# Kernel tuning notes

Hardware: AMD Instinct MI355X
Metric: run time of the kernel (lower is better)

## Reference

```python
import jax, jax.numpy as jnp
import numpy as np

N_NODES = 50000
N_EDGES = 600000
FEAT = 128
HID = 256


def _sage_gcn(feats, src, dst, W, b, n_nodes):
    # DGL SAGEConv aggregator_type='gcn':
    # h_neigh = (sum_{u in N(v)} h_u + h_v) / (in_deg(v) + 1); out = h_neigh @ W + b
    neigh_sum = jax.ops.segment_sum(feats[src], dst, num_segments=n_nodes)  # [N, d]
    in_deg = jax.ops.segment_sum(jnp.ones((src.shape[0],), feats.dtype), dst,
                                 num_segments=n_nodes)  # [N]
    h = (neigh_sum + feats) / (in_deg + 1.0)[:, None]
    return h @ W + b


def setup_inputs() -> dict:
    key = jax.random.key(0)
    ks = jax.random.split(key, 8)
    s = lambda d: 1.0 / np.sqrt(d)
    return {
        "features": jax.random.normal(ks[0], (N_NODES, FEAT), jnp.float32),
        "src": jax.random.randint(ks[1], (N_EDGES,), 0, N_NODES, jnp.int32),
        "dst": jax.random.randint(ks[2], (N_EDGES,), 0, N_NODES, jnp.int32),
        "W1": jax.random.normal(ks[3], (FEAT, HID), jnp.float32) * s(FEAT),
        "b1": jnp.zeros((HID,), jnp.float32),
        "W2": jax.random.normal(ks[4], (HID, HID), jnp.float32) * s(HID),
        "b2": jnp.zeros((HID,), jnp.float32),
        "Wd1": jax.random.normal(ks[5], (HID, HID), jnp.float32) * s(HID),
        "bd1": jnp.zeros((HID,), jnp.float32),
        "Wd2": jax.random.normal(ks[6], (HID, 1), jnp.float32) * s(HID),
        "bd2": jnp.zeros((1,), jnp.float32),
    }


def reference(features, src, dst, W1, b1, W2, b2, Wd1, bd1, Wd2, bd2):
    n = features.shape[0]
    # Encoder: SAGEConv(gcn) -> ReLU -> SAGEConv(gcn)   (dropout inactive in eval)
    h = _sage_gcn(features, src, dst, W1, b1, n)
    h = jax.nn.relu(h)
    h = _sage_gcn(h, src, dst, W2, b2, n)
    # Decoder: Linear -> ReLU -> Linear
    h = jax.nn.relu(h @ Wd1 + bd1)
    return h @ Wd2 + bd2  # [N, 1]
```

## Files before the change

kernel.cpp:

```cpp
#include <hip/hip_runtime.h>
#include <type_traits>

#define NN 50000
#define NE 600000
#define FEAT 128
#define HID 256
#define MAXD 64

typedef float v4f __attribute__((ext_vector_type(4)));
typedef float f32x4 __attribute__((ext_vector_type(4)));
typedef __bf16 bf16x8 __attribute__((ext_vector_type(8)));
using u16 = unsigned short;
using u32 = unsigned int;
typedef u16 u16x4 __attribute__((ext_vector_type(4)));
typedef u16 u16x8 __attribute__((ext_vector_type(8)));

__device__ __forceinline__ u16 f2bf(float f) {
    u32 u = __builtin_bit_cast(u32, f);
    u += 0x7fffu + ((u >> 16) & 1u);
    return (u16)(u >> 16);
}
__device__ __forceinline__ float bf2f(u16 h) {
    u32 u = ((u32)h) << 16;
    return __builtin_bit_cast(float, u);
}

#define NB_FILL 2344
#define NB_CVT 6250
#define NB_W1  128
#define NB_W23 256
__global__ __launch_bounds__(256) void prep_fill_k(const int* __restrict__ src,
                                                   const int* __restrict__ dst,
                                                   int* __restrict__ cnt,
                                                   int* __restrict__ ell,
                                                   const float* __restrict__ feats,
                                                   const float* __restrict__ W1,
                                                   const float* __restrict__ W2,
                                                   const float* __restrict__ Wd1,
                                                   const float* __restrict__ b2,
                                                   u16* __restrict__ featsbf,
                                                   u16* __restrict__ WT1,
                                                   u16* __restrict__ WT23,
                                                   float* __restrict__ c23) {
    int b = blockIdx.x, t = threadIdx.x;
    if (b < NB_FILL) {
        int e = b * 256 + t;
        if (e < NE) {
            int d = dst[e];
            int p = atomicAdd(&cnt[d], 1);
            if (p < MAXD) ell[(size_t)d * MAXD + p] = src[e];
        }
        return;
    }
    b -= NB_FILL;
    if (b < NB_CVT) {
        int i = b * 256 + t;
        v4f v = *(const v4f*)(feats + (size_t)i * 4);
        u16x4 o;
        #pragma unroll
        for (int j = 0; j < 4; j++) o[j] = f2bf(v[j]);
        *(u16x4*)(featsbf + (size_t)i * 4) = o;
    } else if (b < NB_CVT + NB_W1) {
        int idx = (b - NB_CVT) * 256 + t;
        int k = idx >> 8, n = idx & 255;
        WT1[(size_t)n * 128 + k] = f2bf(W1[idx]);
    } else if (b < NB_CVT + NB_W1 + NB_W23) {
        int k = b - NB_CVT - NB_W1;
        int n = t;
        const float* w2row = W2 + (size_t)k * 256;
        float acc = 0.f;
        #pragma unroll 8
        for (int j = 0; j < 256; j++) acc += w2row[j] * Wd1[(size_t)j * 256 + n];
        WT23[(size_t)n * 256 + k] = f2bf(acc);
    } else {
        int n = t;
        float acc = 0.f;
        #pragma unroll 8
        for (int j = 0; j < 256; j++) acc += b2[j] * Wd1[(size_t)j * 256 + n];
        c23[n] = acc;
    }
}

template <int D>
__global__ __launch_bounds__(256) void aggregate_bf_k(const u16* __restrict__ x,
                                                      const int* __restrict__ cnt,
                                                      const int* __restrict__ ell,
                                                      u16* __restrict__ o) {
    constexpr int LPG = (D == 256) ? 32 : 16;
    constexpr int G = 64 / LPG;
    int wave = threadIdx.x >> 6;
    int lane = threadIdx.x & 63;
    int v = blockIdx.x * 4 + wave;
    if (v >= NN) return;
    int g  = lane / LPG;
    int li = lane & (LPG - 1);
    size_t coff = (size_t)li * 8;
    int deg = cnt[v]; if (deg > MAXD) deg = MAXD;
    int cntv = deg + 1;
    const int* cols = ell + (size_t)v * MAXD;
    float acc[8];
    #pragma unroll
    for (int i = 0; i < 8; i++) acc[i] = 0.f;
    int base = 0;
    #pragma unroll 4
    for (; base + G <= cntv; base += G) {
        int idx = base + g;
        int row = (idx < deg) ? cols[idx] : v;
        u16x8 r = *(const u16x8*)(x + (size_t)row * D + coff);
        #pragma unroll
        for (int i = 0; i < 8; i++) acc[i] += bf2f(r[i]);
    }
    if (base + g < cntv) {
        int idx = base + g;
        int row = (idx < deg) ? cols[idx] : v;
        u16x8 r = *(const u16x8*)(x + (size_t)row * D + coff);
        #pragma unroll
        for (int i = 0; i < 8; i++) acc[i] += bf2f(r[i]);
    }
    #pragma unroll
    for (int i = 0; i < 8; i++) {
        acc[i] += __shfl_xor(acc[i], 32, 64);
        if (G == 4) acc[i] += __shfl_xor(acc[i], 16, 64);
    }
    if (lane < LPG) {
        float inv = 1.0f / (float)cntv;
        u16x8 O;
        #pragma unroll
        for (int i = 0; i < 8; i++) O[i] = f2bf(acc[i] * inv);
        *(u16x8*)(o + (size_t)v * D + coff) = O;
    }
}

__global__ __launch_bounds__(256) void agg2_dec_k(const u16* __restrict__ x,
                                                  const int* __restrict__ cnt,
                                                  const int* __restrict__ ell,
                                                  const float* __restrict__ bd1,
                                                  const float* __restrict__ wd2,
                                                  const float* __restrict__ bd2,
                                                  float* __restrict__ out) {
    int wave = threadIdx.x >> 6;
    int lane = threadIdx.x & 63;
    int v = blockIdx.x * 4 + wave;
    if (v >= NN) return;
    int g  = lane >> 5;
    int li = lane & 31;
    size_t coff = (size_t)li * 8;
    int deg = cnt[v]; if (deg > MAXD) deg = MAXD;
    int cntv = deg + 1;
    const int* cols = ell + (size_t)v * MAXD;
    float acc[8];
    #pragma unroll
    for (int i = 0; i < 8; i++) acc[i] = 0.f;
    int base = 0;
    #pragma unroll 4
    for (; base + 2 <= cntv; base += 2) {
        int idx = base + g;
        int row = (idx < deg) ? cols[idx] : v;
        u16x8 r = *(const u16x8*)(x + (size_t)row * 256 + coff);
        #pragma unroll
        for (int i = 0; i < 8; i++) acc[i] += bf2f(r[i]);
    }
    if (base + g < cntv) {
        int idx = base + g;
        int row = (idx < deg) ? cols[idx] : v;
        u16x8 r = *(const u16x8*)(x + (size_t)row * 256 + coff);
        #pragma unroll
        for (int i = 0; i < 8; i++) acc[i] += bf2f(r[i]);
    }
    #pragma unroll
    for (int i = 0; i < 8; i++) acc[i] += __shfl_xor(acc[i], 32, 64);

    float inv = 1.0f / (float)cntv;
    v4f b0 = *(const v4f*)(bd1 + li * 8);
    v4f b1 = *(const v4f*)(bd1 + li * 8 + 4);
    v4f w0 = *(const v4f*)(wd2 + li * 8);
    v4f w1 = *(const v4f*)(wd2 + li * 8 + 4);
    float p = 0.f;
    #pragma unroll
    for (int i = 0; i < 4; i++) p += fmaxf(acc[i] * inv + b0[i], 0.f) * w0[i];
    #pragma unroll
    for (int i = 0; i < 4; i++) p += fmaxf(acc[i + 4] * inv + b1[i], 0.f) * w1[i];
    p += __shfl_xor(p, 1, 64);
    p += __shfl_xor(p, 2, 64);
    p += __shfl_xor(p, 4, 64);
    p += __shfl_xor(p, 8, 64);
    p += __shfl_xor(p, 16, 64);
    if (lane == 0) out[v] = p + bd2[0];
}

#define MFMA_BF16 __builtin_amdgcn_mfma_f32_16x16x32_bf16
#define SW(s, r) (((s) ^ (((r) >> 1) & 3)) * 8)

#define MFMA_STEP(pa0, pa1, pa2, pa3, ph0, ph1)              \
    do {                                                     \
        acc[0][0] = MFMA_BF16(pa0, ph0, acc[0][0], 0, 0, 0); \
        acc[0][1] = MFMA_BF16(pa0, ph1, acc[0][1], 0, 0, 0); \
        acc[1][0] = MFMA_BF16(pa1, ph0, acc[1][0], 0, 0, 0); \
        acc[1][1] = MFMA_BF16(pa1, ph1, acc[1][1], 0, 0, 0); \
        acc[2][0] = MFMA_BF16(pa2, ph0, acc[2][0], 0, 0, 0); \
        acc[2][1] = MFMA_BF16(pa2, ph1, acc[2][1], 0, 0, 0); \
        acc[3][0] = MFMA_BF16(pa3, ph0, acc[3][0], 0, 0, 0); \
        acc[3][1] = MFMA_BF16(pa3, ph1, acc[3][1], 0, 0, 0); \
    } while (0)

__global__ __launch_bounds__(512, 4) void fused_gemm12_k(const u16* __restrict__ A1,
                                                         const u16* __restrict__ B1,
                                                         const float* __restrict__ b1,
                                                         const u16* __restrict__ B23,
                                                         const float* __restrict__ c23,
                                                         u16* __restrict__ Z, int M) {
    __shared__ __attribute__((aligned(16))) u16 sA[2][64 * 32];
    __shared__ __attribute__((aligned(16))) u16 sB[2][256 * 32];
    __shared__ __attribute__((aligned(16))) u16 sH[64 * 264];

    int tid = threadIdx.x;
    int wid = tid >> 6, lane = tid & 63;
    int m0 = blockIdx.x * 64;
    int r16 = lane & 15, sl = lane >> 4, k8 = sl * 8;

    u32 ao[4], bo[2];
    #pragma unroll
    for (int mf = 0; mf < 4; mf++) {
        int ar = mf * 16 + r16;
        ao[mf] = ar * 32 + SW(sl, ar);
    }
    #pragma unroll
    for (int nf = 0; nf < 2; nf++) {
        int bc = wid * 32 + nf * 16 + r16;
        bo[nf] = bc * 32 + SW(sl, bc);
    }

    f32x4 acc[4][2];
    #pragma unroll
    for (int a = 0; a < 4; a++)
        #pragma unroll
        for (int b = 0; b < 2; b++) acc[a][b] = (f32x4)0.f;

    int aRow = tid >> 2, aS = tid & 3;
    u32 aSw = aRow * 32 + SW(aS, aRow);
    int gAr = m0 + aRow; if (gAr >= M) gAr = M - 1;
    const u16* gA = A1 + (size_t)gAr * 128 + aS * 8;
    int bRow[2], bS[2]; u32 bSw[2];
    #pragma unroll
    for (int j = 0; j < 2; j++) {
        int idx = tid + j * 512;
        bRow[j] = idx >> 2; bS[j] = idx & 3;
        bSw[j] = bRow[j] * 32 + SW(bS[j], bRow[j]);
    }

    uint4 rA, rB0, rB1;

    if (tid < 256) rA = *(const uint4*)gA;
    rB0 = *(const uint4*)(B1 + (size_t)bRow[0] * 128 + bS[0] * 8);
    rB1 = *(const uint4*)(B1 + (size_t)bRow[1] * 128 + bS[1] * 8);
    if (tid < 256) *(uint4*)(&sA[0][aSw]) = rA;
    *(uint4*)(&sB[0][bSw[0]]) = rB0;
    *(uint4*)(&sB[0][bSw[1]]) = rB1;
    __syncthreads();

    #pragma unroll
    for (int kb = 0; kb < 4; kb++) {
        int cur = kb & 1;
        if (kb < 3) {
            if (tid < 256) rA = *(const uint4*)(gA + (kb + 1) * 32);
            rB0 = *(const uint4*)(B1 + (size_t)bRow[0] * 128 + (kb + 1) * 32 + bS[0] * 8);
            rB1 = *(const uint4*)(B1 + (size_t)bRow[1] * 128 + (kb + 1) * 32 + bS[1] * 8);
        }
        bf16x8 a0 = *(const bf16x8*)(&sA[cur][ao[0]]);
        bf16x8 a1 = *(const bf16x8*)(&sA[cur][ao[1]]);
        bf16x8 a2 = *(const bf16x8*)(&sA[cur][ao[2]]);
        bf16x8 a3 = *(const bf16x8*)(&sA[cur][ao[3]]);
        bf16x8 h0 = *(const bf16x8*)(&sB[cur][bo[0]]);
        bf16x8 h1 = *(const bf16x8*)(&sB[cur][bo[1]]);
        MFMA_STEP(a0, a1, a2, a3, h0, h1);
        if (kb < 3) {
            int nxt = cur ^ 1;
            if (tid < 256) *(uint4*)(&sA[nxt][aSw]) = rA;
            *(uint4*)(&sB[nxt][bSw[0]]) = rB0;
            *(uint4*)(&sB[nxt][bSw[1]]) = rB1;
        }
        __syncthreads();
    }

    rB0 = *(const uint4*)(B23 + (size_t)bRow[0] * 256 + bS[0] * 8);
    rB1 = *(const uint4*)(B23 + (size_t)bRow[1] * 256 + bS[1] * 8);

    {
        float b1c[2];
        #pragma unroll
        for (int nf = 0; nf < 2; nf++) b1c[nf] = b1[wid * 32 + nf * 16 + r16];
        int rbase = sl * 4;
        #pragma unroll
        for (int mf = 0; mf < 4; mf++)
            #pragma unroll
            for (int j = 0; j < 4; j++) {
                int r = mf * 16 + rbase + j;
                #pragma unroll
                for (int nf = 0; nf < 2; nf++) {
                    int c = wid * 32 + nf * 16 + r16;
                    sH[r * 264 + c] = f2bf(fmaxf(acc[mf][nf][j] + b1c[nf], 0.f));
                }
            }
        #pragma unroll
        for (int a = 0; a < 4; a++)
            #pragma unroll
            for (int b = 0; b < 2; b++) acc[a][b] = (f32x4)0.f;
    }
    *(uint4*)(&sB[0][bSw[0]]) = rB0;
    *(uint4*)(&sB[0][bSw[1]]) = rB1;
    __syncthreads();

    #pragma unroll
    for (int kb = 0; kb < 8; kb++) {
        int cur = kb & 1;
        if (kb < 7) {
            rB0 = *(const uint4*)(B23 + (size_t)bRow[0] * 256 + (kb + 1) * 32 + bS[0] * 8);
            rB1 = *(const uint4*)(B23 + (size_t)bRow[1] * 256 + (kb + 1) * 32 + bS[1] * 8);
        }
        bf16x8 a0 = *(const bf16x8*)(sH + (0 * 16 + r16) * 264 + kb * 32 + k8);
        bf16x8 a1 = *(const bf16x8*)(sH + (1 * 16 + r16) * 264 + kb * 32 + k8);
        bf16x8 a2 = *(const bf16x8*)(sH + (2 * 16 + r16) * 264 + kb * 32 + k8);
        bf16x8 a3 = *(const bf16x8*)(sH + (3 * 16 + r16) * 264 + kb * 32 + k8);
        bf16x8 h0 = *(const bf16x8*)(&sB[cur][bo[0]]);
        bf16x8 h1 = *(const bf16x8*)(&sB[cur][bo[1]]);
        MFMA_STEP(a0, a1, a2, a3, h0, h1);
        if (kb < 7) {
            int nxt = cur ^ 1;
            *(uint4*)(&sB[nxt][bSw[0]]) = rB0;
            *(uint4*)(&sB[nxt][bSw[1]]) = rB1;
        }
        __syncthreads();
    }

    {
        float cc[2];
        #pragma unroll
        for (int nf = 0; nf < 2; nf++) cc[nf] = c23[wid * 32 + nf * 16 + r16];
        int rbase = sl * 4;
        #pragma unroll
        for (int mf = 0; mf < 4; mf++)
            #pragma unroll
            for (int j = 0; j < 4; j++) {
                int gr = m0 + mf * 16 + rbase + j;
                if (gr < M) {
                    #pragma unroll
                    for (int nf = 0; nf < 2; nf++) {
                        int gc = wid * 32 + nf * 16 + r16;
                        Z[(size_t)gr * 256 + gc] = f2bf(acc[mf][nf][j] + cc[nf]);
                    }
                }
            }
    }
}

extern "C" void kernel_launch(void* const* d_in, const int* in_sizes, int n_in,
                              void* d_out, int out_size, void* d_ws, size_t ws_size,
                              hipStream_t stream) {
    const float* feats = (const float*)d_in[0];
    const int*   src   = (const int*)d_in[1];
    const int*   dst   = (const int*)d_in[2];
    const float* W1    = (const float*)d_in[3];
    const float* b1    = (const float*)d_in[4];
    const float* W2    = (const float*)d_in[5];
    const float* b2    = (const float*)d_in[6];
    const float* Wd1   = (const float*)d_in[7];
    const float* bd1   = (const float*)d_in[8];
    const float* Wd2   = (const float*)d_in[9];
    const float* bd2   = (const float*)d_in[10];
    float* out = (float*)d_out;

    char* base = (char*)d_ws;
    size_t off = 0;
    int* cnt = (int*)(base + off); off += (size_t)NN * 4;
    int* ell = (int*)(base + off); off += (size_t)NN * MAXD * 4;
    u16* WT1   = (u16*)(base + off); off += (size_t)FEAT * 256 * 2;
    u16* WT23  = (u16*)(base + off); off += (size_t)HID * 256 * 2;
    float* c23 = (float*)(base + off); off += 256 * 4;
    off = (off + 255) & ~(size_t)255;
    u16* featsbf = (u16*)(base + off); off += (size_t)NN * FEAT * 2;
    u16* A1      = (u16*)(base + off); off += (size_t)NN * FEAT * 2;
    u16* Zbf     = (u16*)(base + off); off += (size_t)NN * HID * 2;

    hipMemsetAsync(cnt, 0, (size_t)NN * 4, stream);
    prep_fill_k<<<NB_FILL + NB_CVT + NB_W1 + NB_W23 + 1, 256, 0, stream>>>(
        src, dst, cnt, ell, feats, W1, W2, Wd1, b2, featsbf, WT1, WT23, c23);

    aggregate_bf_k<FEAT><<<(NN + 3) / 4, 256, 0, stream>>>(featsbf, cnt, ell, A1);

    fused_gemm12_k<<<(NN + 63) / 64, 512, 0, stream>>>(A1, WT1, b1, WT23, c23,
                                                       Zbf, NN);

    agg2_dec_k<<<(NN + 3) / 4, 256, 0, stream>>>(Zbf, cnt, ell, bd1, Wd2, bd2, out);
}
```

Measured before the change: 157.4 us.

## Store ELL neighbor indices as u16 and split W2·Wd1 fold into its own kernel

The ELL neighbor list is stored as 16-bit indices instead of 32-bit, which is valid because the node count fits in u16. This halves index traffic in the fill and in both aggregation kernels. The edge-fill blocks now handle 4 edges per thread. The W2·Wd1 weight fold moves out of the prep kernel into a dedicated kernel that stages 4 W2 rows in shared memory, so each Wd1 load is reused across 4 outputs. The trade-off is an extra kernel launch, and that fold no longer overlaps with the fill work.

```diff
diff --git a/kernel.cpp b/kernel.cpp
--- a/kernel.cpp
+++ b/kernel.cpp
@@ -25,30 +25,28 @@
     return __builtin_bit_cast(float, u);
 }
 
-#define NB_FILL 2344
+#define NB_FILL 586
 #define NB_CVT 6250
 #define NB_W1  128
-#define NB_W23 256
 __global__ __launch_bounds__(256) void prep_fill_k(const int* __restrict__ src,
                                                    const int* __restrict__ dst,
                                                    int* __restrict__ cnt,
-                                                   int* __restrict__ ell,
+                                                   u16* __restrict__ ell,
                                                    const float* __restrict__ feats,
                                                    const float* __restrict__ W1,
-                                                   const float* __restrict__ W2,
-                                                   const float* __restrict__ Wd1,
-                                                   const float* __restrict__ b2,
                                                    u16* __restrict__ featsbf,
-                                                   u16* __restrict__ WT1,
-                                                   u16* __restrict__ WT23,
-                                                   float* __restrict__ c23) {
+                                                   u16* __restrict__ WT1) {
     int b = blockIdx.x, t = threadIdx.x;
     if (b < NB_FILL) {
-        int e = b * 256 + t;
-        if (e < NE) {
-            int d = dst[e];
-            int p = atomicAdd(&cnt[d], 1);
-            if (p < MAXD) ell[(size_t)d * MAXD + p] = src[e];
+        int ebase = b * 1024 + t;
+        #pragma unroll
+        for (int i = 0; i < 4; i++) {
+            int e = ebase + i * 256;
+            if (e < NE) {
+                int d = dst[e];
+                int p = atomicAdd(&cnt[d], 1);
+                if (p < MAXD) ell[(size_t)d * MAXD + p] = (u16)src[e];
+            }
         }
         return;
     }
@@ -60,31 +58,43 @@
         #pragma unroll
         for (int j = 0; j < 4; j++) o[j] = f2bf(v[j]);
         *(u16x4*)(featsbf + (size_t)i * 4) = o;
-    } else if (b < NB_CVT + NB_W1) {
+    } else {
         int idx = (b - NB_CVT) * 256 + t;
         int k = idx >> 8, n = idx & 255;
         WT1[(size_t)n * 128 + k] = f2bf(W1[idx]);
-    } else if (b < NB_CVT + NB_W1 + NB_W23) {
-        int k = b - NB_CVT - NB_W1;
-        int n = t;
-        const float* w2row = W2 + (size_t)k * 256;
-        float acc = 0.f;
-        #pragma unroll 8
-        for (int j = 0; j < 256; j++) acc += w2row[j] * Wd1[(size_t)j * 256 + n];
-        WT23[(size_t)n * 256 + k] = f2bf(acc);
-    } else {
-        int n = t;
-        float acc = 0.f;
-        #pragma unroll 8
-        for (int j = 0; j < 256; j++) acc += b2[j] * Wd1[(size_t)j * 256 + n];
-        c23[n] = acc;
-    }
+    }
+}
+
+__global__ __launch_bounds__(256) void w23_k(const float* __restrict__ W2,
+                                             const float* __restrict__ Wd1,
+                                             const float* __restrict__ b2,
+                                             u16* __restrict__ WT23,
+                                             float* __restrict__ c23) {
+    __shared__ float w2s[4][256];
+    int t = threadIdx.x;
+    int k0 = blockIdx.x * 4;
+    #pragma unroll
+    for (int r = 0; r < 4; r++) w2s[r][t] = W2[(size_t)(k0 + r) * 256 + t];
+    __syncthreads();
+    float acc[4] = {0.f, 0.f, 0.f, 0.f};
+    float accc = 0.f;
+    bool doC = (blockIdx.x == 0);
+    #pragma unroll 4
+    for (int j = 0; j < 256; j++) {
+        float w = Wd1[(size_t)j * 256 + t];
+        #pragma unroll
+        for (int r = 0; r < 4; r++) acc[r] += w2s[r][j] * w;
+        if (doC) accc += b2[j] * w;
+    }
+    #pragma unroll
+    for (int r = 0; r < 4; r++) WT23[(size_t)t * 256 + k0 + r] = f2bf(acc[r]);
+    if (doC) c23[t] = accc;
 }
 
 template <int D>
 __global__ __launch_bounds__(256) void aggregate_bf_k(const u16* __restrict__ x,
                                                       const int* __restrict__ cnt,
-                                                      const int* __restrict__ ell,
+                                                      const u16* __restrict__ ell,
                                                       u16* __restrict__ o) {
     constexpr int LPG = (D == 256) ? 32 : 16;
     constexpr int G = 64 / LPG;
@@ -97,7 +107,7 @@
     size_t coff = (size_t)li * 8;
     int deg = cnt[v]; if (deg > MAXD) deg = MAXD;
     int cntv = deg + 1;
-    const int* cols = ell + (size_t)v * MAXD;
+    const u16* cols = ell + (size_t)v * MAXD;
     float acc[8];
     #pragma unroll
     for (int i = 0; i < 8; i++) acc[i] = 0.f;
@@ -105,14 +115,14 @@
     #pragma unroll 4
     for (; base + G <= cntv; base += G) {
         int idx = base + g;
-        int row = (idx < deg) ? cols[idx] : v;
+        int row = (idx < deg) ? (int)cols[idx] : v;
         u16x8 r = *(const u16x8*)(x + (size_t)row * D + coff);
         #pragma unroll
         for (int i = 0; i < 8; i++) acc[i] += bf2f(r[i]);
     }
     if (base + g < cntv) {
         int idx = base + g;
-        int row = (idx < deg) ? cols[idx] : v;
+        int row = (idx < deg) ? (int)cols[idx] : v;
         u16x8 r = *(const u16x8*)(x + (size_t)row * D + coff);
         #pragma unroll
         for (int i = 0; i < 8; i++) acc[i] += bf2f(r[i]);
@@ -133,7 +143,7 @@
 
 __global__ __launch_bounds__(256) void agg2_dec_k(const u16* __restrict__ x,
                                                   const int* __restrict__ cnt,
-                                                  const int* __restrict__ ell,
+                                                  const u16* __restrict__ ell,
                                                   const float* __restrict__ bd1,
                                                   const float* __restrict__ wd2,
                                                   const float* __restrict__ bd2,
@@ -147,7 +157,7 @@
     size_t coff = (size_t)li * 8;
     int deg = cnt[v]; if (deg > MAXD) deg = MAXD;
     int cntv = deg + 1;
-    const int* cols = ell + (size_t)v * MAXD;
+    const u16* cols = ell + (size_t)v * MAXD;
     float acc[8];
     #pragma unroll
     for (int i = 0; i < 8; i++) acc[i] = 0.f;
@@ -155,14 +165,14 @@
     #pragma unroll 4
     for (; base + 2 <= cntv; base += 2) {
         int idx = base + g;
-        int row = (idx < deg) ? cols[idx] : v;
+        int row = (idx < deg) ? (int)cols[idx] : v;
         u16x8 r = *(const u16x8*)(x + (size_t)row * 256 + coff);
         #pragma unroll
         for (int i = 0; i < 8; i++) acc[i] += bf2f(r[i]);
     }
     if (base + g < cntv) {
         int idx = base + g;
-        int row = (idx < deg) ? cols[idx] : v;
+        int row = (idx < deg) ? (int)cols[idx] : v;
         u16x8 r = *(const u16x8*)(x + (size_t)row * 256 + coff);
         #pragma unroll
         for (int i = 0; i < 8; i++) acc[i] += bf2f(r[i]);
@@ -372,7 +382,7 @@
     char* base = (char*)d_ws;
     size_t off = 0;
     int* cnt = (int*)(base + off); off += (size_t)NN * 4;
-    int* ell = (int*)(base + off); off += (size_t)NN * MAXD * 4;
+    u16* ell = (u16*)(base + off); off += (size_t)NN * MAXD * 2;
     u16* WT1   = (u16*)(base + off); off += (size_t)FEAT * 256 * 2;
     u16* WT23  = (u16*)(base + off); off += (size_t)HID * 256 * 2;
     float* c23 = (float*)(base + off); off += 256 * 4;
@@ -382,8 +392,10 @@
     u16* Zbf     = (u16*)(base + off); off += (size_t)NN * HID * 2;
 
     hipMemsetAsync(cnt, 0, (size_t)NN * 4, stream);
-    prep_fill_k<<<NB_FILL + NB_CVT + NB_W1 + NB_W23 + 1, 256, 0, stream>>>(
-        src, dst, cnt, ell, feats, W1, W2, Wd1, b2, featsbf, WT1, WT23, c23);
+    prep_fill_k<<<NB_FILL + NB_CVT + NB_W1, 256, 0, stream>>>(
+        src, dst, cnt, ell, feats, W1, featsbf, WT1);
+
+    w23_k<<<64, 256, 0, stream>>>(W2, Wd1, b2, WT23, c23);
 
     aggregate_bf_k<FEAT><<<(NN + 3) / 4, 256, 0, stream>>>(featsbf, cnt, ell, A1);
 
```

New measurement: 175.7 us. 11.6% more time.
